# Optimization experiments

Measured on AMD Instinct MI355X. Metric: run time of the kernel, lower is better.

The kernel has to match this reference:

```python
import jax, jax.numpy as jnp
import numpy as np
from jax import lax

B, IMG = 2, 512
FMC, HID, A, NC = 1024, 512, 9, 21
RED, POOL, TOP, IOU_THR = 16, 7, 20, 0.3
NEG = -1e30
# 3 scales x 3 aspect ratios (w, h)
ANCHOR_WH = np.array([[s * np.sqrt(r), s / np.sqrt(r)] for s in (64.0, 128.0, 256.0) for r in (0.5, 1.0, 2.0)], dtype=np.float32)


def conv(x, w, b, stride, pad):
    y = lax.conv_general_dilated(x, w, (stride, stride), pad, dimension_numbers=('NCHW', 'OIHW', 'NCHW'))
    return y + b[None, :, None, None]


def make_anchors(H, W, stride):
    cy = (jnp.arange(H, dtype=jnp.float32) + 0.5) * stride
    cx = (jnp.arange(W, dtype=jnp.float32) + 0.5) * stride
    cyg, cxg = jnp.meshgrid(cy, cx, indexing='ij')  # [H,W]
    wh = jnp.asarray(ANCHOR_WH)  # [A,2]
    w2 = wh[None, None, :, 0] / 2
    h2 = wh[None, None, :, 1] / 2
    cxg = cxg[:, :, None]
    cyg = cyg[:, :, None]
    boxes = jnp.stack([cxg - w2, cyg - h2, cxg + w2, cyg + h2], axis=-1)  # [H,W,A,4]
    return boxes.reshape(-1, 4)


def box_iou(b, boxes):
    # b [4], boxes [N,4], (x1,y1,x2,y2)
    ix1 = jnp.maximum(b[0], boxes[:, 0])
    iy1 = jnp.maximum(b[1], boxes[:, 1])
    ix2 = jnp.minimum(b[2], boxes[:, 2])
    iy2 = jnp.minimum(b[3], boxes[:, 3])
    inter = jnp.maximum(ix2 - ix1, 0.0) * jnp.maximum(iy2 - iy1, 0.0)
    ab = jnp.maximum(b[2] - b[0], 0.0) * jnp.maximum(b[3] - b[1], 0.0)
    ar = jnp.maximum(boxes[:, 2] - boxes[:, 0], 0.0) * jnp.maximum(boxes[:, 3] - boxes[:, 1], 0.0)
    return inter / (ab + ar - inter + 1e-8)


def nms_one(boxes, scores):
    # greedy NMS, fixed TOP selections
    n = scores.shape[0]
    idxs = jnp.arange(n)

    def step(s, _):
        i = jnp.argmax(s)
        b, sc = boxes[i], s[i]
        s = jnp.where((box_iou(b, boxes) > IOU_THR) | (idxs == i), NEG, s)
        return s, (b, sc)

    _, (bs, ss) = lax.scan(step, scores, None, length=TOP)
    return bs, ss  # [TOP,4], [TOP]


def roi_align_one(fm_b, boxes):
    # fm_b [C,H,W], boxes [R,4] in image coords -> [R,C,POOL,POOL]
    C, H, W = fm_b.shape
    b = boxes / RED
    t = (jnp.arange(POOL, dtype=jnp.float32) + 0.5) / POOL
    xs = b[:, 0:1] + jnp.maximum(b[:, 2] - b[:, 0], 0.0)[:, None] * t[None]  # [R,P]
    ys = b[:, 1:2] + jnp.maximum(b[:, 3] - b[:, 1], 0.0)[:, None] * t[None]
    x = jnp.clip(xs[:, None, :], 0.0, W - 1.0) * jnp.ones((1, POOL, 1), jnp.float32)  # [R,P,P]
    y = jnp.clip(ys[:, :, None], 0.0, H - 1.0) * jnp.ones((1, 1, POOL), jnp.float32)
    x0f, y0f = jnp.floor(x), jnp.floor(y)
    x0, y0 = x0f.astype(jnp.int32), y0f.astype(jnp.int32)
    x1 = jnp.minimum(x0 + 1, W - 1)
    y1 = jnp.minimum(y0 + 1, H - 1)
    lx, ly = x - x0f, y - y0f
    v00 = fm_b[:, y0, x0]
    v01 = fm_b[:, y0, x1]
    v10 = fm_b[:, y1, x0]
    v11 = fm_b[:, y1, x1]  # [C,R,P,P]
    out = v00 * (1 - ly) * (1 - lx) + v01 * (1 - ly) * lx + v10 * ly * (1 - lx) + v11 * ly * lx
    return out.transpose(1, 0, 2, 3)


def setup_inputs() -> dict:
    key = jax.random.key(0)
    ks = jax.random.split(key, 16)
    s = 0.02
    return {
        'img': jax.random.normal(ks[0], (B, 3, IMG, IMG), jnp.float32),
        'img_id': jnp.arange(B, dtype=jnp.int32),
        'cnn_w': jax.random.normal(ks[1], (FMC, 3, RED, RED), jnp.float32) * s,
        'cnn_b': jnp.zeros((FMC,), jnp.float32),
        'rpn_w': jax.random.normal(ks[2], (HID, FMC, 3, 3), jnp.float32) * s,
        'rpn_b': jnp.zeros((HID,), jnp.float32),
        'rpn_reg_w': jax.random.normal(ks[3], (A * 4, HID, 1, 1), jnp.float32) * s,
        'rpn_reg_b': jnp.zeros((A * 4,), jnp.float32),
        'rpn_cls_w': jax.random.normal(ks[4], (A, HID, 1, 1), jnp.float32) * s,
        'rpn_cls_b': jnp.zeros((A,), jnp.float32),
        'fc_w': jax.random.normal(ks[5], (FMC * POOL * POOL, 1024), jnp.float32) * 0.005,
        'fc_b': jnp.zeros((1024,), jnp.float32),
        'reg_w': jax.random.normal(ks[6], (1024, 4), jnp.float32) * s,
        'reg_b': jnp.zeros((4,), jnp.float32),
        'cls_w': jax.random.normal(ks[7], (1024, NC), jnp.float32) * s,
        'cls_b': jnp.zeros((NC,), jnp.float32),
    }


def reference(img, img_id, cnn_w, cnn_b, rpn_w, rpn_b, rpn_reg_w, rpn_reg_b, rpn_cls_w, rpn_cls_b, fc_w, fc_b, reg_w, reg_b, cls_w, cls_b):
    fm = jax.nn.relu(conv(img, cnn_w, cnn_b, RED, 'VALID'))  # [B,1024,32,32]
    Bn, C, H, W = fm.shape
    # sliding-window(3x3, stride 1) + per-slice RPN == 3x3 SAME conv + 1x1 heads
    h = jax.nn.relu(conv(fm, rpn_w, rpn_b, 1, 'SAME'))
    rpn_reg = conv(h, rpn_reg_w, rpn_reg_b, 1, 'SAME').transpose(0, 2, 3, 1).reshape(Bn, -1, 4)  # (h,w,a) order
    rpn_cls = conv(h, rpn_cls_w, rpn_cls_b, 1, 'SAME').transpose(0, 2, 3, 1).reshape(Bn, -1)
    anchors = make_anchors(H, W, RED)  # [H*W*A,4]
    nms_reg, nms_cls = jax.vmap(nms_one)(rpn_reg + anchors[None], rpn_cls)  # [B,TOP,4],[B,TOP]
    pooled = jax.vmap(roi_align_one)(fm[img_id], nms_reg)  # [B,TOP,C,P,P]
    flat = pooled.reshape(Bn * TOP, -1)
    hf = jax.nn.relu(flat @ fc_w + fc_b)
    rcnn_reg = (hf @ reg_w + reg_b).reshape(Bn, -1, 4)
    rcnn_cls = (hf @ cls_w + cls_b).reshape(Bn, TOP, -1)
    return rpn_reg, rpn_cls, nms_reg, nms_cls, rcnn_reg, rcnn_cls, anchors
```

## Files before the change

kernel.cpp:

```cpp
#include <hip/hip_runtime.h>
#include <math.h>


#define NEGV (-1e30f)

typedef unsigned short u16;
typedef float v4f __attribute__((ext_vector_type(4)));
typedef short short8 __attribute__((ext_vector_type(8)));

#define O_RPN_REG 0
#define O_RPN_CLS 73728
#define O_NMS_REG 92160
#define O_NMS_CLS 92320
#define O_RCNN_REG 92360
#define O_RCNN_CLS 92520
#define O_ANCH 93360

#define W_FM   0u
#define W_ZERO 2097152u
#define W_PROP 3145728u
#define W_SCR  3219456u
#define W_FLAT 3237888u
#define W_HF   5244928u
#define W_A1H  5285888u
#define W_A1L  6072320u
#define W_B1H  6858752u
#define W_B1L  7251968u
#define W_FMH  7645184u
#define W_FML  8693760u
#define W_B2H  9742336u
#define W_B2L  12101632u
#define W_PART 14460928u

static __device__ __forceinline__ float relu_(float v) { return fmaxf(v, 0.0f); }

static __device__ __forceinline__ void gload16(const void* g, void* l) {
    __builtin_amdgcn_global_load_lds(
        (const __attribute__((address_space(1))) unsigned int*)g,
        (__attribute__((address_space(3))) unsigned int*)l, 16, 0, 0);
}

static __device__ __forceinline__ u16 bf16_rtne(float x) {
    unsigned int u = __float_as_uint(x);
    unsigned int r = u + 0x7fffu + ((u >> 16) & 1u);
    return (u16)(r >> 16);
}
static __device__ __forceinline__ void split2(float x, u16& h, u16& l) {
    h = bf16_rtne(x);
    const float hf = __uint_as_float(((unsigned int)h) << 16);
    l = bf16_rtne(x - hf);
}
static __device__ __forceinline__ void split8_store(const float* v, u16* dsth, u16* dstl) {
    uint4 H, Lo;
    u16 h0, l0, h1, l1;
    split2(v[0], h0, l0); split2(v[1], h1, l1);
    H.x = (unsigned)h0 | ((unsigned)h1 << 16); Lo.x = (unsigned)l0 | ((unsigned)l1 << 16);
    split2(v[2], h0, l0); split2(v[3], h1, l1);
    H.y = (unsigned)h0 | ((unsigned)h1 << 16); Lo.y = (unsigned)l0 | ((unsigned)l1 << 16);
    split2(v[4], h0, l0); split2(v[5], h1, l1);
    H.z = (unsigned)h0 | ((unsigned)h1 << 16); Lo.z = (unsigned)l0 | ((unsigned)l1 << 16);
    split2(v[6], h0, l0); split2(v[7], h1, l1);
    H.w = (unsigned)h0 | ((unsigned)h1 << 16); Lo.w = (unsigned)l0 | ((unsigned)l1 << 16);
    *(uint4*)dsth = H; *(uint4*)dstl = Lo;
}

static __device__ __forceinline__ void anchor_wh(int a, float& w2, float& h2) {
    double s = (a < 3) ? 64.0 : (a < 6) ? 128.0 : 256.0;
    int rm = a - (a / 3) * 3;
    double r = (rm == 0) ? 0.5 : (rm == 1) ? 1.0 : 2.0;
    double sq = sqrt(r);
    w2 = (float)(s * sq) * 0.5f;
    h2 = (float)(s / sq) * 0.5f;
}

__global__ void k_prep_a1(const float* __restrict__ img, u16* __restrict__ a1h, u16* __restrict__ a1l,
                          float* __restrict__ zbuf) {
    if (blockIdx.x == 0 && threadIdx.x < 64) zbuf[threadIdx.x] = 0.0f;
    const int idx = blockIdx.x * 256 + threadIdx.x;
    const int m = idx / 192, kq = (idx - m * 192) * 4;
    const int b = m >> 10, i = (m >> 5) & 31, j = m & 31;
    const int c = kq >> 8, rem = kq & 255, y = rem >> 4, x = rem & 15;
    const float4 v = *(const float4*)(img + ((size_t)((b * 3 + c) * 512 + i * 16 + y)) * 512 + j * 16 + x);
    ushort4 H, Lo;
    split2(v.x, H.x, Lo.x); split2(v.y, H.y, Lo.y);
    split2(v.z, H.z, Lo.z); split2(v.w, H.w, Lo.w);
    *(ushort4*)(a1h + (size_t)idx * 4) = H;
    *(ushort4*)(a1l + (size_t)idx * 4) = Lo;
}

__global__ void k_split4(const float* __restrict__ src, u16* __restrict__ h, u16* __restrict__ l, int n4) {
    const int idx = blockIdx.x * 256 + threadIdx.x;
    if (idx >= n4) return;
    const float4 v = *(const float4*)(src + (size_t)idx * 4);
    ushort4 H, Lo;
    split2(v.x, H.x, Lo.x); split2(v.y, H.y, Lo.y);
    split2(v.z, H.z, Lo.z); split2(v.w, H.w, Lo.w);
    *(ushort4*)(h + (size_t)idx * 4) = H;
    *(ushort4*)(l + (size_t)idx * 4) = Lo;
}

__global__ void k_prep_w2(const float* __restrict__ w, u16* __restrict__ bh, u16* __restrict__ bl) {
    const int idx = blockIdx.x * 256 + threadIdx.x;
    const int oc = idx / 2304, r = idx - oc * 2304, d = r >> 8, ic4 = (r & 255) * 4;
    const float* p = w + (size_t)oc * 9216 + (size_t)ic4 * 9 + d;
    float4 v; v.x = p[0]; v.y = p[9]; v.z = p[18]; v.w = p[27];
    ushort4 H, Lo;
    split2(v.x, H.x, Lo.x); split2(v.y, H.y, Lo.y);
    split2(v.z, H.z, Lo.z); split2(v.w, H.w, Lo.w);
    const size_t o = (size_t)oc * 9216 + d * 1024 + ic4;
    *(ushort4*)(bh + o) = H;
    *(ushort4*)(bl + o) = Lo;
}

template<int MODE>
__global__ __launch_bounds__(256, 3) void k_gemm(
        const u16* __restrict__ Agh, const u16* __restrict__ Agl,
        const u16* __restrict__ Bgh, const u16* __restrict__ Bgl,
        const float* __restrict__ bias, float* __restrict__ Cout, float* __restrict__ Cout2,
        const int KA, const int KB, const int nchunk, const int ldc, const int do_bias_relu,
        u16* __restrict__ outH, u16* __restrict__ outL, const float* __restrict__ zbuf) {
    __shared__ __align__(16) u16 AsH[2 * 128 * 32];
    __shared__ __align__(16) u16 AsL[2 * 128 * 32];
    __shared__ __align__(16) u16 BsH[2 * 64 * 32];
    __shared__ __align__(16) u16 BsL[2 * 64 * 32];
    const int tid = threadIdx.x;
    const int w = tid >> 6, L = tid & 63;
    const int q = L >> 4, lr = L & 15;
    const int wm = w >> 1, wn = w & 1;
    const int m0 = blockIdx.x * 128, n0 = blockIdx.y * 64;
    const int zbase = blockIdx.z * nchunk;
    float* C;
    if (MODE == 1) {
        C = (blockIdx.z < 4) ? (Cout + (size_t)blockIdx.z * (2048u * 512u))
                             : (Cout2 + (size_t)(blockIdx.z - 4) * (2048u * 512u));
    } else {
        C = Cout;
    }
    const int seg = L & 3, rsub = L >> 2;

    u16* lseg[6];
    int lsz[6];
    const u16* gbase[6];
    int arow_b[6], arow_i[6], arow_j[6];
    int kindv[6];
#pragma unroll
    for (int s = 0; s < 6; ++s) {
        const int idx = w * 6 + s;
        int kind, inst;
        if (idx < 8)       { kind = 0; inst = idx; }
        else if (idx < 16) { kind = 1; inst = idx - 8; }
        else if (idx < 20) { kind = 2; inst = idx - 16; }
        else               { kind = 3; inst = idx - 20; }
        kindv[s] = kind;
        const int r = inst * 16 + rsub;
        u16* lb = (kind == 0) ? AsH : (kind == 1) ? AsL : (kind == 2) ? BsH : BsL;
        lseg[s] = lb + r * 32 + seg * 8;
        lsz[s] = (kind < 2) ? (128 * 32) : (64 * 32);
        arow_b[s] = 0; arow_i[s] = 0; arow_j[s] = 0;
        if (kind >= 2) {
            const u16* gb = (kind == 2) ? Bgh : Bgl;
            gbase[s] = gb + (size_t)(n0 + r) * KB + seg * 8;
        } else if (MODE == 0) {
            const u16* gb = (kind == 0) ? Agh : Agl;
            gbase[s] = gb + (size_t)(m0 + r) * KA + seg * 8;
        } else {
            const int m = m0 + r;
            arow_b[s] = m >> 10; arow_i[s] = (m >> 5) & 31; arow_j[s] = m & 31;
            gbase[s] = (kind == 0) ? Agh : Agl;
        }
    }

    v4f acc[4][2];
#pragma unroll
    for (int t = 0; t < 4; ++t)
#pragma unroll
        for (int u2 = 0; u2 < 2; ++u2) acc[t][u2] = (v4f){0.f, 0.f, 0.f, 0.f};

#define ISSUE(c_, bb_) do { \
    int d_, ic_, kB_; \
    if (MODE == 0) { kB_ = (c_) * 32; d_ = 0; ic_ = kB_; } \
    else { const int g_ = zbase + (c_); d_ = g_ >> 5; ic_ = (g_ & 31) << 5; kB_ = d_ * 1024 + ic_; } \
    const int di_ = d_ / 3, dj_ = d_ - di_ * 3; \
    _Pragma("unroll") \
    for (int s = 0; s < 6; ++s) { \
        const u16* gsrc_; \
        if (kindv[s] >= 2) gsrc_ = gbase[s] + kB_; \
        else if (MODE == 0) gsrc_ = gbase[s] + ic_; \
        else { \
            const int y_ = arow_i[s] + di_ - 1, x_ = arow_j[s] + dj_ - 1; \
            const bool ok_ = ((unsigned)y_ < 32u) && ((unsigned)x_ < 32u); \
            const int yc_ = ok_ ? y_ : 0, xc_ = ok_ ? x_ : 0; \
            const u16* ga_ = gbase[s] + (size_t)((arow_b[s] * 32 + yc_) * 32 + xc_) * 1024 + ic_ + seg * 8; \
            gsrc_ = ok_ ? ga_ : (const u16*)zbuf; \
        } \
        gload16(gsrc_, lseg[s] + (bb_) * lsz[s]); \
    } \
} while (0)

    int cur = 0;
    ISSUE(0, 0);
    for (int c = 0; c < nchunk; ++c) {
        __syncthreads();
        if (c + 1 < nchunk) ISSUE(c + 1, cur ^ 1);
        const int ao = cur * (128 * 32), bo = cur * (64 * 32);
        short8 ah[4], al[4], bh[2], bl[2];
#pragma unroll
        for (int t = 0; t < 4; ++t) {
            ah[t] = *(const short8*)(AsH + ao + (wm * 64 + t * 16 + lr) * 32 + q * 8);
            al[t] = *(const short8*)(AsL + ao + (wm * 64 + t * 16 + lr) * 32 + q * 8);
        }
#pragma unroll
        for (int u2 = 0; u2 < 2; ++u2) {
            bh[u2] = *(const short8*)(BsH + bo + (wn * 32 + u2 * 16 + lr) * 32 + q * 8);
            bl[u2] = *(const short8*)(BsL + bo + (wn * 32 + u2 * 16 + lr) * 32 + q * 8);
        }
#pragma unroll
        for (int t = 0; t < 4; ++t)
#pragma unroll
            for (int u2 = 0; u2 < 2; ++u2) {
                acc[t][u2] = __builtin_amdgcn_mfma_f32_16x16x32_bf16(ah[t], bh[u2], acc[t][u2], 0, 0, 0);
                acc[t][u2] = __builtin_amdgcn_mfma_f32_16x16x32_bf16(ah[t], bl[u2], acc[t][u2], 0, 0, 0);
                acc[t][u2] = __builtin_amdgcn_mfma_f32_16x16x32_bf16(al[t], bh[u2], acc[t][u2], 0, 0, 0);
            }
        cur ^= 1;
    }
#undef ISSUE

#pragma unroll
    for (int t = 0; t < 4; ++t) {
        const int row = m0 + wm * 64 + t * 16 + q * 4;
#pragma unroll
        for (int u2 = 0; u2 < 2; ++u2) {
            const int col = n0 + wn * 32 + u2 * 16 + lr;
            const float bv = do_bias_relu ? bias[col] : 0.f;
#pragma unroll
            for (int r = 0; r < 4; ++r) {
                float vv = acc[t][u2][r];
                if (do_bias_relu) vv = relu_(vv + bv);
                C[(size_t)(row + r) * ldc + col] = vv;
                if (MODE == 0 && outH != nullptr) {
                    u16 hh, ll; split2(vv, hh, ll);
                    outH[(size_t)(row + r) * 1024 + col] = hh;
                    outL[(size_t)(row + r) * 1024 + col] = ll;
                }
            }
        }
    }
}

__global__ __launch_bounds__(64) void k_rpn_heads(const float* __restrict__ partA,
        const float* __restrict__ partB,
        const float* __restrict__ rpnb,
        const float* __restrict__ regw, const float* __restrict__ regb,
        const float* __restrict__ clsw, const float* __restrict__ clsb,
        float* __restrict__ out, float* __restrict__ prop, float* __restrict__ scr) {
    __shared__ __align__(16) float hrow[512];
    const int m = blockIdx.x, tid = threadIdx.x;
    const int b = m >> 10, qd = m & 1023, ii = qd >> 5, jj = qd & 31;
    for (int i = tid * 4; i < 512; i += 256) {
        const size_t ro = (size_t)m * 512 + i;
        const float4 a0 = *(const float4*)(partA + ro);
        const float4 a1 = *(const float4*)(partA + 1048576u + ro);
        const float4 a2 = *(const float4*)(partA + 2097152u + ro);
        const float4 a3 = *(const float4*)(partA + 3145728u + ro);
        const float4 a4 = *(const float4*)(partB + ro);
        const float4 a5 = *(const float4*)(partB + 1048576u + ro);
        const float4 bb = *(const float4*)(rpnb + i);
        float4 o;
        o.x = relu_(a0.x + a1.x + a2.x + a3.x + a4.x + a5.x + bb.x);
        o.y = relu_(a0.y + a1.y + a2.y + a3.y + a4.y + a5.y + bb.y);
        o.z = relu_(a0.z + a1.z + a2.z + a3.z + a4.z + a5.z + bb.z);
        o.w = relu_(a0.w + a1.w + a2.w + a3.w + a4.w + a5.w + bb.w);
        *(float4*)&hrow[i] = o;
    }
    __syncthreads();
    if (tid < 45) {
        const int isreg = (tid < 36);
        const float* wp = isreg ? (regw + (size_t)tid * 512) : (clsw + (size_t)(tid - 36) * 512);
        float acc2 = isreg ? regb[tid] : clsb[tid - 36];
        for (int k = 0; k < 512; k += 4) {
            const float4 wv = *(const float4*)(wp + k);
            acc2 += hrow[k + 0] * wv.x; acc2 += hrow[k + 1] * wv.y;
            acc2 += hrow[k + 2] * wv.z; acc2 += hrow[k + 3] * wv.w;
        }
        if (isreg) {
            out[O_RPN_REG + (size_t)b * 36864 + qd * 36 + tid] = acc2;
            const int a = tid >> 2, cc = tid & 3;
            float w2, h2; anchor_wh(a, w2, h2);
            const float cx = ((float)jj + 0.5f) * 16.f, cy = ((float)ii + 0.5f) * 16.f;
            const float av = (cc == 0) ? cx - w2 : (cc == 1) ? cy - h2 : (cc == 2) ? cx + w2 : cy + h2;
            prop[(size_t)b * 36864 + qd * 36 + tid] = acc2 + av;
        } else {
            const int n = tid - 36;
            out[O_RPN_CLS + (size_t)b * 9216 + qd * 9 + n] = acc2;
            scr[(size_t)b * 9216 + qd * 9 + n] = acc2;
        }
    }
    if (b == 0 && tid >= 48 && tid < 57) {
        const int a = tid - 48;
        float w2, h2; anchor_wh(a, w2, h2);
        const float cx = ((float)jj + 0.5f) * 16.f, cy = ((float)ii + 0.5f) * 16.f;
        const float4 av4 = make_float4(cx - w2, cy - h2, cx + w2, cy + h2);
        *(float4*)(out + O_ANCH + (size_t)(qd * 9 + a) * 4) = av4;
    }
}

__global__ __launch_bounds__(512) void k_nms3(const float* __restrict__ prop,
        const float* __restrict__ scr, float* __restrict__ out) {
    __shared__ float wv_[2][8];
    __shared__ int wi_[2][8];
    const int b = blockIdx.x, tid = threadIdx.x;
    const int lane = tid & 63, wid = tid >> 6;
    const float* P = prop + (size_t)b * 36864;
    float4 bx[18]; float sv[18];
#pragma unroll
    for (int k = 0; k < 18; ++k) {
        const int i = tid * 18 + k;
        bx[k] = *(const float4*)(P + (size_t)i * 4);
        sv[k] = scr[b * 9216 + i];
    }
    for (int t = 0; t < 20; ++t) {
        float bv = -3.4e38f; int bi = 0;
#pragma unroll
        for (int k = 0; k < 18; ++k)
            if (sv[k] > bv) { bv = sv[k]; bi = tid * 18 + k; }
#pragma unroll
        for (int off = 1; off < 64; off <<= 1) {
            const float ov = __shfl_xor(bv, off);
            const int oi = __shfl_xor(bi, off);
            if (ov > bv || (ov == bv && oi < bi)) { bv = ov; bi = oi; }
        }
        if (lane == 0) { wv_[t & 1][wid] = bv; wi_[t & 1][wid] = bi; }
        __syncthreads();
        float rb = wv_[t & 1][0]; int sel = wi_[t & 1][0];
#pragma unroll
        for (int j = 1; j < 8; ++j) {
            const float v2 = wv_[t & 1][j]; const int i2 = wi_[t & 1][j];
            if (v2 > rb || (v2 == rb && i2 < sel)) { rb = v2; sel = i2; }
        }
        const float4 bb = *(const float4*)(P + (size_t)sel * 4);
        if (tid == 0) {
            *(float4*)(out + O_NMS_REG + (size_t)(b * 20 + t) * 4) = bb;
            out[O_NMS_CLS + b * 20 + t] = rb;
        }
        const float ab2 = fmaxf(bb.z - bb.x, 0.f) * fmaxf(bb.w - bb.y, 0.f);
#pragma unroll
        for (int k = 0; k < 18; ++k) {
            const float ix1 = fmaxf(bb.x, bx[k].x), iy1 = fmaxf(bb.y, bx[k].y);
            const float ix2 = fminf(bb.z, bx[k].z), iy2 = fminf(bb.w, bx[k].w);
            const float inter = fmaxf(ix2 - ix1, 0.f) * fmaxf(iy2 - iy1, 0.f);
            const float ar2 = fmaxf(bx[k].z - bx[k].x, 0.f) * fmaxf(bx[k].w - bx[k].y, 0.f);
            const float iou = inter / (ab2 + ar2 - inter + 1e-8f);
            if (iou > 0.3f || (tid * 18 + k) == sel) sv[k] = NEGV;
        }
    }
}

__global__ __launch_bounds__(256) void k_roi(const float* __restrict__ fm,
        const int* __restrict__ img_id, const float* __restrict__ nreg,
        float* __restrict__ flat) {
    const int py = blockIdx.x, roi = blockIdx.y, b = blockIdx.z;
    const float* bx = nreg + (size_t)(b * 20 + roi) * 4;
    const float b0 = bx[0] * 0.0625f, b1 = bx[1] * 0.0625f;
    const float b2 = bx[2] * 0.0625f, b3 = bx[3] * 0.0625f;
    const float wd = fmaxf(b2 - b0, 0.f), hg = fmaxf(b3 - b1, 0.f);
    const float tyv = ((float)py + 0.5f) / 7.0f;
    const float ycv = fminf(fmaxf(b1 + hg * tyv, 0.f), 31.f);
    const float y0f = floorf(ycv);
    const int y0 = (int)y0f, y1 = min(y0 + 1, 31);
    const float ly = ycv - y0f, omly = 1.f - ly;
    const int bb = img_id[b];
    const float* fmb = fm + (size_t)bb * (32 * 32 * 1024);
    const size_t orow = (size_t)(b * 20 + roi) * 50176 + (size_t)py * 7;
    for (int px = 0; px < 7; ++px) {
        const float txv = ((float)px + 0.5f) / 7.0f;
        const float xcv = fminf(fmaxf(b0 + wd * txv, 0.f), 31.f);
        const float x0f = floorf(xcv);
        const int x0 = (int)x0f, x1 = min(x0 + 1, 31);
        const float lx = xcv - x0f, omlx = 1.f - lx;
        const int o00 = ((y0 * 32) + x0) << 10, o01 = ((y0 * 32) + x1) << 10;
        const int o10 = ((y1 * 32) + x0) << 10, o11 = ((y1 * 32) + x1) << 10;
        for (int u = 0; u < 4; ++u) {
            const int c = threadIdx.x + u * 256;
            const float v00 = fmb[o00 + c], v01 = fmb[o01 + c];
            const float v10 = fmb[o10 + c], v11 = fmb[o11 + c];
            const float val = ((v00 * omly) * omlx) + ((v01 * omly) * lx)
                            + ((v10 * ly) * omlx) + ((v11 * ly) * lx);
            flat[orow + (size_t)c * 49 + px] = val;
        }
    }
}

__global__ void k_hf_init(const float* __restrict__ fcb, float* __restrict__ hf) {
    const int i = blockIdx.x * 256 + threadIdx.x;
    if (i < 40 * 1024) hf[i] = fcb[i & 1023];
}

__global__ __launch_bounds__(256, 2) void k_fc_mfma(const float* __restrict__ flat,
        const float* __restrict__ fcw, float* __restrict__ hf) {
    __shared__ __align__(16) u16 AsH[4 * 48 * 8];
    __shared__ __align__(16) u16 AsL[4 * 48 * 8];
    __shared__ __align__(16) u16 BsH[4 * 256 * 8];
    __shared__ __align__(16) u16 BsL[4 * 256 * 8];
    const int tid = threadIdx.x;
    const int w = tid >> 6, L = tid & 63, q = L >> 4, lr = L & 15;
    const int n0 = blockIdx.x * 256, kb = blockIdx.y * 512;
    if (tid < 32) {
        const int oct = tid >> 3, m = 40 + (tid & 7);
        *(uint4*)(AsH + (oct * 48 + m) * 8) = make_uint4(0, 0, 0, 0);
        *(uint4*)(AsL + (oct * 48 + m) * 8) = make_uint4(0, 0, 0, 0);
    }
    const int am = tid >> 2, aoct = tid & 3;
    const float* abase = flat + (size_t)am * 50176 + kb + aoct * 8;
    const float* bcol = fcw + n0 + tid;

    v4f acc[3][4];
#pragma unroll
    for (int mt = 0; mt < 3; ++mt)
#pragma unroll
        for (int nt = 0; nt < 4; ++nt) acc[mt][nt] = (v4f){0.f, 0.f, 0.f, 0.f};

    float areg[8];
    float breg[4][8];

#define LOADF(c_) do { \
    if (tid < 160) { \
        const float4 u_ = *(const float4*)(abase + (c_) * 32); \
        const float4 v_ = *(const float4*)(abase + (c_) * 32 + 4); \
        areg[0] = u_.x; areg[1] = u_.y; areg[2] = u_.z; areg[3] = u_.w; \
        areg[4] = v_.x; areg[5] = v_.y; areg[6] = v_.z; areg[7] = v_.w; \
    } \
    _Pragma("unroll") \
    for (int o_ = 0; o_ < 4; ++o_) \
        _Pragma("unroll") \
        for (int j_ = 0; j_ < 8; ++j_) \
            breg[o_][j_] = bcol[(size_t)(kb + (c_) * 32 + o_ * 8 + j_) * 1024]; \
} while (0)

    LOADF(0);
    for (int c = 0; c < 16; ++c) {
        __syncthreads();
        if (tid < 160)
            split8_store(areg, AsH + (aoct * 48 + am) * 8, AsL + (aoct * 48 + am) * 8);
#pragma unroll
        for (int o = 0; o < 4; ++o)
            split8_store(breg[o], BsH + (o * 256 + tid) * 8, BsL + (o * 256 + tid) * 8);
        __syncthreads();
        if (c + 1 < 16) LOADF(c + 1);
        short8 ah[3], al[3], bh2[4], bl2[4];
#pragma unroll
        for (int mt = 0; mt < 3; ++mt) {
            ah[mt] = *(const short8*)(AsH + (q * 48 + mt * 16 + lr) * 8);
            al[mt] = *(const short8*)(AsL + (q * 48 + mt * 16 + lr) * 8);
        }
#pragma unroll
        for (int nt = 0; nt < 4; ++nt) {
            bh2[nt] = *(const short8*)(BsH + (q * 256 + w * 64 + nt * 16 + lr) * 8);
            bl2[nt] = *(const short8*)(BsL + (q * 256 + w * 64 + nt * 16 + lr) * 8);
        }
#pragma unroll
        for (int mt = 0; mt < 3; ++mt)
#pragma unroll
            for (int nt = 0; nt < 4; ++nt) {
                acc[mt][nt] = __builtin_amdgcn_mfma_f32_16x16x32_bf16(ah[mt], bh2[nt], acc[mt][nt], 0, 0, 0);
                acc[mt][nt] = __builtin_amdgcn_mfma_f32_16x16x32_bf16(ah[mt], bl2[nt], acc[mt][nt], 0, 0, 0);
                acc[mt][nt] = __builtin_amdgcn_mfma_f32_16x16x32_bf16(al[mt], bh2[nt], acc[mt][nt], 0, 0, 0);
            }
    }
#undef LOADF

#pragma unroll
    for (int mt = 0; mt < 3; ++mt) {
#pragma unroll
        for (int nt = 0; nt < 4; ++nt) {
#pragma unroll
            for (int r = 0; r < 4; ++r) {
                const int row = mt * 16 + q * 4 + r;
                if (row < 40)
                    atomicAdd(hf + (size_t)row * 1024 + n0 + w * 64 + nt * 16 + lr, acc[mt][nt][r]);
            }
        }
    }
}

__global__ __launch_bounds__(64) void k_heads(const float* __restrict__ hf,
        const float* __restrict__ regw, const float* __restrict__ regb,
        const float* __restrict__ clsw, const float* __restrict__ clsb,
        float* __restrict__ out) {
    __shared__ __align__(16) float hrow[1024];
    const int m = blockIdx.x, tid = threadIdx.x;
    for (int i = tid * 4; i < 1024; i += 256) {
        const float4 v = *(const float4*)(hf + (size_t)m * 1024 + i);
        hrow[i + 0] = relu_(v.x); hrow[i + 1] = relu_(v.y);
        hrow[i + 2] = relu_(v.z); hrow[i + 3] = relu_(v.w);
    }
    __syncthreads();
    if (tid < 25) {
        float acc2 = 0.f;
        if (tid < 4) {
            for (int k = 0; k < 1024; ++k) acc2 += hrow[k] * regw[(size_t)k * 4 + tid];
            out[O_RCNN_REG + m * 4 + tid] = acc2 + regb[tid];
        } else {
            const int n = tid - 4;
            for (int k = 0; k < 1024; ++k) acc2 += hrow[k] * clsw[(size_t)k * 21 + n];
            out[O_RCNN_CLS + m * 21 + n] = acc2 + clsb[n];
        }
    }
}

extern "C" void kernel_launch(void* const* d_in, const int* in_sizes, int n_in,
                              void* d_out, int out_size, void* d_ws, size_t ws_size,
                              hipStream_t stream) {
    (void)in_sizes; (void)n_in; (void)out_size; (void)ws_size;
    const float* img       = (const float*)d_in[0];
    const int*   img_id    = (const int*)  d_in[1];
    const float* cnn_w     = (const float*)d_in[2];
    const float* cnn_b     = (const float*)d_in[3];
    const float* rpn_w     = (const float*)d_in[4];
    const float* rpn_b     = (const float*)d_in[5];
    const float* rpn_reg_w = (const float*)d_in[6];
    const float* rpn_reg_b = (const float*)d_in[7];
    const float* rpn_cls_w = (const float*)d_in[8];
    const float* rpn_cls_b = (const float*)d_in[9];
    const float* fc_w      = (const float*)d_in[10];
    const float* fc_b      = (const float*)d_in[11];
    const float* reg_w     = (const float*)d_in[12];
    const float* reg_b     = (const float*)d_in[13];
    const float* cls_w     = (const float*)d_in[14];
    const float* cls_b     = (const float*)d_in[15];
    float* out = (float*)d_out;
    float* ws  = (float*)d_ws;

    float* fm   = ws + W_FM;
    float* zbuf = ws + W_ZERO;
    float* prop = ws + W_PROP;
    float* scr  = ws + W_SCR;
    float* flat = ws + W_FLAT;
    float* hf   = ws + W_HF;
    u16* a1h = (u16*)(ws + W_A1H);
    u16* a1l = (u16*)(ws + W_A1L);
    u16* b1h = (u16*)(ws + W_B1H);
    u16* b1l = (u16*)(ws + W_B1L);
    u16* fmh = (u16*)(ws + W_FMH);
    u16* fml = (u16*)(ws + W_FML);
    u16* b2h = (u16*)(ws + W_B2H);
    u16* b2l = (u16*)(ws + W_B2L);
    float* partA = ws + W_FLAT;
    float* partB = ws + W_PART;

    k_prep_a1<<<1536, 256, 0, stream>>>(img, a1h, a1l, zbuf);
    k_split4<<<768, 256, 0, stream>>>(cnn_w, b1h, b1l, 196608);
    k_prep_w2<<<4608, 256, 0, stream>>>(rpn_w, b2h, b2l);
    k_gemm<0><<<dim3(16, 16, 1), 256, 0, stream>>>(a1h, a1l, b1h, b1l, cnn_b, fm, nullptr,
                                                   768, 768, 24, 1024, 1, fmh, fml, zbuf);
    k_gemm<1><<<dim3(16, 8, 6), 256, 0, stream>>>(fmh, fml, b2h, b2l, nullptr, partA, partB,
                                                  1024, 9216, 48, 512, 0, nullptr, nullptr, zbuf);
    k_rpn_heads<<<2048, 64, 0, stream>>>(partA, partB, rpn_b, rpn_reg_w, rpn_reg_b, rpn_cls_w, rpn_cls_b,
                                         out, prop, scr);
    k_nms3<<<2, 512, 0, stream>>>(prop, scr, out);
    k_roi<<<dim3(7, 20, 2), 256, 0, stream>>>(fm, img_id, out + O_NMS_REG, flat);
    k_hf_init<<<160, 256, 0, stream>>>(fc_b, hf);
    k_fc_mfma<<<dim3(4, 98), 256, 0, stream>>>(flat, fc_w, hf);
    k_heads<<<40, 64, 0, stream>>>(hf, reg_w, reg_b, cls_w, cls_b, out);
}
```

Measured before the change: 623.1 us.

## Split-K first conv GEMM, stage weight transpose and ROI output through LDS

The first conv GEMM now runs as a two-way split-K over blockIdx.z, with partial sums written to separate buffers. A new reduce kernel then adds the partials, applies bias and ReLU, and produces the hi/lo bf16 split. The RPN weight prep loads each output channel coalesced into shared memory before transposing, and ROI align now stages each (roi, 256-channel) tile in LDS so the flat output is written with coalesced float4 stores. This trades an extra kernel launch and extra partial-buffer traffic for more GEMM parallelism and better memory coalescing.

```diff
diff --git a/kernel.cpp b/kernel.cpp
--- a/kernel.cpp
+++ b/kernel.cpp
@@ -99,17 +99,33 @@
     *(ushort4*)(l + (size_t)idx * 4) = Lo;
 }
 
-__global__ void k_prep_w2(const float* __restrict__ w, u16* __restrict__ bh, u16* __restrict__ bl) {
-    const int idx = blockIdx.x * 256 + threadIdx.x;
-    const int oc = idx / 2304, r = idx - oc * 2304, d = r >> 8, ic4 = (r & 255) * 4;
-    const float* p = w + (size_t)oc * 9216 + (size_t)ic4 * 9 + d;
-    float4 v; v.x = p[0]; v.y = p[9]; v.z = p[18]; v.w = p[27];
-    ushort4 H, Lo;
-    split2(v.x, H.x, Lo.x); split2(v.y, H.y, Lo.y);
-    split2(v.z, H.z, Lo.z); split2(v.w, H.w, Lo.w);
-    const size_t o = (size_t)oc * 9216 + d * 1024 + ic4;
-    *(ushort4*)(bh + o) = H;
-    *(ushort4*)(bl + o) = Lo;
+__global__ __launch_bounds__(256) void k_prep_w2(const float* __restrict__ w,
+        u16* __restrict__ bh, u16* __restrict__ bl) {
+    __shared__ __align__(16) u16 sh[9216];
+    __shared__ __align__(16) u16 sl[9216];
+    const int oc = blockIdx.x;
+    const float* p = w + (size_t)oc * 9216;
+    for (int i = threadIdx.x * 4; i < 9216; i += 1024) {
+        const float4 v = *(const float4*)(p + i);
+        ushort4 H, Lo;
+        split2(v.x, H.x, Lo.x); split2(v.y, H.y, Lo.y);
+        split2(v.z, H.z, Lo.z); split2(v.w, H.w, Lo.w);
+        *(ushort4*)(sh + i) = H;
+        *(ushort4*)(sl + i) = Lo;
+    }
+    __syncthreads();
+    const int ic4 = threadIdx.x * 4;
+#pragma unroll
+    for (int d = 0; d < 9; ++d) {
+        ushort4 H, Lo;
+        H.x = sh[(ic4 + 0) * 9 + d]; Lo.x = sl[(ic4 + 0) * 9 + d];
+        H.y = sh[(ic4 + 1) * 9 + d]; Lo.y = sl[(ic4 + 1) * 9 + d];
+        H.z = sh[(ic4 + 2) * 9 + d]; Lo.z = sl[(ic4 + 2) * 9 + d];
+        H.w = sh[(ic4 + 3) * 9 + d]; Lo.w = sl[(ic4 + 3) * 9 + d];
+        const size_t o = (size_t)oc * 9216 + d * 1024 + ic4;
+        *(ushort4*)(bh + o) = H;
+        *(ushort4*)(bl + o) = Lo;
+    }
 }
 
 template<int MODE>
@@ -134,7 +150,7 @@
         C = (blockIdx.z < 4) ? (Cout + (size_t)blockIdx.z * (2048u * 512u))
                              : (Cout2 + (size_t)(blockIdx.z - 4) * (2048u * 512u));
     } else {
-        C = Cout;
+        C = (blockIdx.z == 0) ? Cout : Cout2;
     }
     const int seg = L & 3, rsub = L >> 2;
 
@@ -178,7 +194,7 @@
 
 #define ISSUE(c_, bb_) do { \
     int d_, ic_, kB_; \
-    if (MODE == 0) { kB_ = (c_) * 32; d_ = 0; ic_ = kB_; } \
+    if (MODE == 0) { const int g_ = zbase + (c_); kB_ = g_ * 32; d_ = 0; ic_ = kB_; } \
     else { const int g_ = zbase + (c_); d_ = g_ >> 5; ic_ = (g_ & 31) << 5; kB_ = d_ * 1024 + ic_; } \
     const int di_ = d_ / 3, dj_ = d_ - di_ * 3; \
     _Pragma("unroll") \
@@ -246,6 +262,24 @@
             }
         }
     }
+}
+
+__global__ void k_c1_reduce(const float* __restrict__ p1, const float* __restrict__ cb,
+                            float* __restrict__ fm, u16* __restrict__ fmh, u16* __restrict__ fml) {
+    const size_t o = ((size_t)blockIdx.x * 256 + threadIdx.x) * 4;
+    float4 a = *(const float4*)(fm + o);
+    const float4 b4 = *(const float4*)(p1 + o);
+    const float4 bb = *(const float4*)(cb + (o & 1023));
+    a.x = relu_(a.x + b4.x + bb.x);
+    a.y = relu_(a.y + b4.y + bb.y);
+    a.z = relu_(a.z + b4.z + bb.z);
+    a.w = relu_(a.w + b4.w + bb.w);
+    *(float4*)(fm + o) = a;
+    ushort4 H, Lo;
+    split2(a.x, H.x, Lo.x); split2(a.y, H.y, Lo.y);
+    split2(a.z, H.z, Lo.z); split2(a.w, H.w, Lo.w);
+    *(ushort4*)(fmh + o) = H;
+    *(ushort4*)(fml + o) = Lo;
 }
 
 __global__ __launch_bounds__(64) void k_rpn_heads(const float* __restrict__ partA,
@@ -359,36 +393,41 @@
 __global__ __launch_bounds__(256) void k_roi(const float* __restrict__ fm,
         const int* __restrict__ img_id, const float* __restrict__ nreg,
         float* __restrict__ flat) {
-    const int py = blockIdx.x, roi = blockIdx.y, b = blockIdx.z;
+    __shared__ float tile[12544];
+    const int c0 = blockIdx.x * 256;
+    const int roi = blockIdx.y, b = blockIdx.z;
     const float* bx = nreg + (size_t)(b * 20 + roi) * 4;
     const float b0 = bx[0] * 0.0625f, b1 = bx[1] * 0.0625f;
     const float b2 = bx[2] * 0.0625f, b3 = bx[3] * 0.0625f;
     const float wd = fmaxf(b2 - b0, 0.f), hg = fmaxf(b3 - b1, 0.f);
-    const float tyv = ((float)py + 0.5f) / 7.0f;
-    const float ycv = fminf(fmaxf(b1 + hg * tyv, 0.f), 31.f);
-    const float y0f = floorf(ycv);
-    const int y0 = (int)y0f, y1 = min(y0 + 1, 31);
-    const float ly = ycv - y0f, omly = 1.f - ly;
     const int bb = img_id[b];
     const float* fmb = fm + (size_t)bb * (32 * 32 * 1024);
-    const size_t orow = (size_t)(b * 20 + roi) * 50176 + (size_t)py * 7;
-    for (int px = 0; px < 7; ++px) {
-        const float txv = ((float)px + 0.5f) / 7.0f;
-        const float xcv = fminf(fmaxf(b0 + wd * txv, 0.f), 31.f);
-        const float x0f = floorf(xcv);
-        const int x0 = (int)x0f, x1 = min(x0 + 1, 31);
-        const float lx = xcv - x0f, omlx = 1.f - lx;
-        const int o00 = ((y0 * 32) + x0) << 10, o01 = ((y0 * 32) + x1) << 10;
-        const int o10 = ((y1 * 32) + x0) << 10, o11 = ((y1 * 32) + x1) << 10;
-        for (int u = 0; u < 4; ++u) {
-            const int c = threadIdx.x + u * 256;
+    const int c = c0 + threadIdx.x;
+    for (int py = 0; py < 7; ++py) {
+        const float tyv = ((float)py + 0.5f) / 7.0f;
+        const float ycv = fminf(fmaxf(b1 + hg * tyv, 0.f), 31.f);
+        const float y0f = floorf(ycv);
+        const int y0 = (int)y0f, y1 = min(y0 + 1, 31);
+        const float ly = ycv - y0f, omly = 1.f - ly;
+        for (int px = 0; px < 7; ++px) {
+            const float txv = ((float)px + 0.5f) / 7.0f;
+            const float xcv = fminf(fmaxf(b0 + wd * txv, 0.f), 31.f);
+            const float x0f = floorf(xcv);
+            const int x0 = (int)x0f, x1 = min(x0 + 1, 31);
+            const float lx = xcv - x0f, omlx = 1.f - lx;
+            const int o00 = ((y0 * 32) + x0) << 10, o01 = ((y0 * 32) + x1) << 10;
+            const int o10 = ((y1 * 32) + x0) << 10, o11 = ((y1 * 32) + x1) << 10;
             const float v00 = fmb[o00 + c], v01 = fmb[o01 + c];
             const float v10 = fmb[o10 + c], v11 = fmb[o11 + c];
-            const float val = ((v00 * omly) * omlx) + ((v01 * omly) * lx)
-                            + ((v10 * ly) * omlx) + ((v11 * ly) * lx);
-            flat[orow + (size_t)c * 49 + px] = val;
-        }
-    }
+            tile[threadIdx.x * 49 + py * 7 + px] =
+                ((v00 * omly) * omlx) + ((v01 * omly) * lx)
+                + ((v10 * ly) * omlx) + ((v11 * ly) * lx);
+        }
+    }
+    __syncthreads();
+    const size_t ob = (size_t)(b * 20 + roi) * 50176 + (size_t)c0 * 49;
+    for (int i = threadIdx.x * 4; i < 12544; i += 1024)
+        *(float4*)(flat + ob + i) = *(const float4*)&tile[i];
 }
 
 __global__ void k_hf_init(const float* __restrict__ fcb, float* __restrict__ hf) {
@@ -550,15 +589,16 @@
 
     k_prep_a1<<<1536, 256, 0, stream>>>(img, a1h, a1l, zbuf);
     k_split4<<<768, 256, 0, stream>>>(cnn_w, b1h, b1l, 196608);
-    k_prep_w2<<<4608, 256, 0, stream>>>(rpn_w, b2h, b2l);
-    k_gemm<0><<<dim3(16, 16, 1), 256, 0, stream>>>(a1h, a1l, b1h, b1l, cnn_b, fm, nullptr,
-                                                   768, 768, 24, 1024, 1, fmh, fml, zbuf);
+    k_prep_w2<<<512, 256, 0, stream>>>(rpn_w, b2h, b2l);
+    k_gemm<0><<<dim3(16, 16, 2), 256, 0, stream>>>(a1h, a1l, b1h, b1l, cnn_b, fm, partB,
+                                                   768, 768, 12, 1024, 0, nullptr, nullptr, zbuf);
+    k_c1_reduce<<<2048, 256, 0, stream>>>(partB, cnn_b, fm, fmh, fml);
     k_gemm<1><<<dim3(16, 8, 6), 256, 0, stream>>>(fmh, fml, b2h, b2l, nullptr, partA, partB,
                                                   1024, 9216, 48, 512, 0, nullptr, nullptr, zbuf);
     k_rpn_heads<<<2048, 64, 0, stream>>>(partA, partB, rpn_b, rpn_reg_w, rpn_reg_b, rpn_cls_w, rpn_cls_b,
                                          out, prop, scr);
     k_nms3<<<2, 512, 0, stream>>>(prop, scr, out);
-    k_roi<<<dim3(7, 20, 2), 256, 0, stream>>>(fm, img_id, out + O_NMS_REG, flat);
+    k_roi<<<dim3(4, 20, 2), 256, 0, stream>>>(fm, img_id, out + O_NMS_REG, flat);
     k_hf_init<<<160, 256, 0, stream>>>(fc_b, hf);
     k_fc_mfma<<<dim3(4, 98), 256, 0, stream>>>(flat, fc_w, hf);
     k_heads<<<40, 64, 0, stream>>>(hf, reg_w, reg_b, cls_w, cls_b, out);
```

Measured after the change: 593.2 us. 1.05x faster.
